# Kernel optimization log

Hardware: AMD Instinct MI355X
Metric: run time of the kernel (lower is better)

## Reference

```python
import jax, jax.numpy as jnp
import numpy as np

B, N, F_IN = 8, 2048, 16
E, H = 64, 4
D = E // H
HID, A = 128, 4
QUEUE_IDX = np.array([0, 1, 2, 3, 6, 7, 8, 9, 10, 11, 12, 13])


def setup_inputs() -> dict:
    key = jax.random.key(0)
    ks = iter(jax.random.split(key, 64))
    def g(*s, scale=0.05):
        return jax.random.normal(next(ks), s, jnp.float32) * scale
    inp = {}
    inp['node_features'] = jax.random.normal(next(ks), (B, N, F_IN), jnp.float32) * 10.0
    inp['adjacency'] = jax.random.randint(next(ks), (B, N, N), 0, 2).astype(jnp.float32)
    for i, fin in enumerate([F_IN, E]):
        inp[f'l{i}_wq'] = g(fin, E)
        inp[f'l{i}_wk'] = g(fin, E)
        inp[f'l{i}_wv'] = g(fin, E)
        inp[f'l{i}_in_w'] = g(E, 3 * E)
        inp[f'l{i}_in_b'] = jnp.zeros(3 * E, jnp.float32)
        inp[f'l{i}_mha_ow'] = g(E, E)
        inp[f'l{i}_mha_ob'] = jnp.zeros(E, jnp.float32)
        inp[f'l{i}_op_w'] = g(E, E)
        inp[f'l{i}_op_b'] = jnp.zeros(E, jnp.float32)
    inp['head_w1'] = g(E, HID)
    inp['head_b1'] = jnp.zeros(HID, jnp.float32)
    inp['head_w2'] = g(HID, HID)
    inp['head_b2'] = jnp.zeros(HID, jnp.float32)
    inp['head_w3'] = g(HID, A, scale=0.001)
    inp['head_b3'] = jnp.zeros(A, jnp.float32)
    return inp


def _gat_layer(x, mask, wq, wk, wv, in_w, in_b, mow, mob, opw, opb):
    # x: [B,N,Fin], mask: [B,N,N] bool (True = blocked)
    b, n, _ = x.shape
    q = x @ wq  # layer's own Q/K/V projections (bias-free)
    k = x @ wk
    v = x @ wv
    # nn.MultiheadAttention's internal in_proj (with bias)
    Q = q @ in_w[:, :E] + in_b[:E]
    K = k @ in_w[:, E:2 * E] + in_b[E:2 * E]
    V = v @ in_w[:, 2 * E:] + in_b[2 * E:]
    Qh = Q.reshape(b, n, H, D)
    Kh = K.reshape(b, n, H, D)
    Vh = V.reshape(b, n, H, D)
    s = jnp.einsum('bqhd,bkhd->bhqk', Qh, Kh) / jnp.sqrt(jnp.float32(D))
    s = jnp.where(mask[:, None, :, :], -jnp.inf, s)
    a = jax.nn.softmax(s, axis=-1)  # diagonal always unmasked -> no all-inf rows
    o = jnp.einsum('bhqk,bkhd->bqhd', a, Vh).reshape(b, n, E)
    o = o @ mow + mob  # MHA out_proj
    return o @ opw + opb  # layer out_proj


def reference(node_features, adjacency,
              l0_wq, l0_wk, l0_wv, l0_in_w, l0_in_b, l0_mha_ow, l0_mha_ob, l0_op_w, l0_op_b,
              l1_wq, l1_wk, l1_wv, l1_in_w, l1_in_b, l1_mha_ow, l1_mha_ob, l1_op_w, l1_op_b,
              head_w1, head_b1, head_w2, head_b2, head_w3, head_b3):
    f = node_features.shape[-1]
    scale = jnp.ones(f, node_features.dtype).at[QUEUE_IDX].set(1.0 / 50.0).at[5].set(1.0 / 300.0)
    x = node_features * scale
    n = adjacency.shape[-1]
    mask = (adjacency + jnp.eye(n, dtype=adjacency.dtype)) == 0
    x = jax.nn.relu(_gat_layer(x, mask, l0_wq, l0_wk, l0_wv, l0_in_w, l0_in_b, l0_mha_ow, l0_mha_ob, l0_op_w, l0_op_b))
    x = jax.nn.relu(_gat_layer(x, mask, l1_wq, l1_wk, l1_wv, l1_in_w, l1_in_b, l1_mha_ow, l1_mha_ob, l1_op_w, l1_op_b))
    h = jax.nn.relu(x @ head_w1 + head_b1)
    h = jax.nn.relu(h @ head_w2 + head_b2)
    return h @ head_w3 + head_b3  # [B, N, n_actions]
```

## Files before the change

### kernel.cpp

```cpp
#include <hip/hip_runtime.h>

#define BB 8
#define NN 2048
#define FIN0 16
#define EE 64
#define HH 4
#define DD 16
#define HIDN 128
#define AA 4

__global__ __launch_bounds__(256) void k_mask(const float* __restrict__ adj, unsigned long long* __restrict__ mbT) {
    const int ITER = 32;
    for (int it = 0; it < ITER; it++) {
        long long idx = ((long long)blockIdx.x * ITER + it) * 256 + threadIdx.x;
        int k = (int)(idx & (NN - 1));
        int r = (int)((idx >> 11) & (NN - 1));
        int b = (int)(idx >> 22);
        float a = adj[idx];
        bool blocked = (a == 0.0f) && (k != r);
        unsigned long long m = __ballot(blocked);
        if ((threadIdx.x & 63) == 0) mbT[((long long)b * 32 + (k >> 6)) * NN + r] = m;
    }
}

#define QSCALE 0.36067376022224085f
__device__ __forceinline__ float sfeat(int f) {
    return (f == 4 || f == 14 || f == 15) ? 1.0f : ((f == 5) ? (1.0f / 300.0f) : 0.02f);
}
__global__ __launch_bounds__(256) void k_wcomb(
        const float* __restrict__ wq0, const float* __restrict__ wk0, const float* __restrict__ wv0,
        const float* __restrict__ inw0, const float* __restrict__ inb0,
        const float* __restrict__ mow0, const float* __restrict__ mob0,
        const float* __restrict__ opw0, const float* __restrict__ opb0,
        const float* __restrict__ wq1, const float* __restrict__ wk1, const float* __restrict__ wv1,
        const float* __restrict__ inw1, const float* __restrict__ inb1,
        const float* __restrict__ mow1, const float* __restrict__ mob1,
        const float* __restrict__ opw1, const float* __restrict__ opb1,
        float* __restrict__ CW0, float* __restrict__ WO0, float* __restrict__ bO0, float* __restrict__ bQ0,
        float* __restrict__ CW1, float* __restrict__ WO1, float* __restrict__ bO1, float* __restrict__ bQ1) {
    int ly = blockIdx.y;
    int fin = ly ? EE : FIN0;
    const float* wq = ly ? wq1 : wq0; const float* wk = ly ? wk1 : wk0; const float* wv = ly ? wv1 : wv0;
    const float* inw = ly ? inw1 : inw0; const float* inb = ly ? inb1 : inb0;
    const float* mow = ly ? mow1 : mow0; const float* mob = ly ? mob1 : mob0;
    const float* opw = ly ? opw1 : opw0; const float* opb = ly ? opb1 : opb0;
    float* CW = ly ? CW1 : CW0; float* WO = ly ? WO1 : WO0;
    float* bO = ly ? bO1 : bO0; float* bQ = ly ? bQ1 : bQ0;

    int t = blockIdx.x * 256 + threadIdx.x;
    int t1 = fin * 192;
    int t2 = t1 + 4096;
    int t3 = t2 + 64;
    int t4 = t3 + 192;
    if (t < t1) {
        int f = t / 192, j = t % 192;
        const float* w = (j < 64) ? wq : ((j < 128) ? wk : wv);
        float acc = 0.f;
        for (int kk = 0; kk < 64; kk++) acc += w[f * 64 + kk] * inw[kk * 192 + j];
        if (j < 64) acc *= QSCALE;
        if (ly == 0) acc *= sfeat(f);
        CW[t] = acc;
    } else if (t < t2) {
        int u = t - t1; int i = u >> 6, j = u & 63;
        float acc = 0.f;
        for (int kk = 0; kk < 64; kk++) acc += mow[i * 64 + kk] * opw[kk * 64 + j];
        WO[u] = acc;
    } else if (t < t3) {
        int j = t - t2;
        float acc = opb[j];
        for (int kk = 0; kk < 64; kk++) acc += mob[kk] * opw[kk * 64 + j];
        bO[j] = acc;
    } else if (t < t4) {
        int j = t - t3;
        bQ[j] = inb[j] * ((j < 64) ? QSCALE : 1.0f);
    }
}

template <int FINP>
__global__ __launch_bounds__(256) void k_qkv(const float* __restrict__ X, const float* __restrict__ CW,
                                             const float* __restrict__ bQ,
                                             float* __restrict__ Q, float* __restrict__ K, float* __restrict__ V) {
    int lane = threadIdx.x & 63;
    int quarter = threadIdx.x >> 6;
    int row = blockIdx.x * 64 + lane;
    int b = row >> 11, n = row & (NN - 1);
    float xr[FINP];
    const float4* xp = (const float4*)(X + (long long)row * FINP);
#pragma unroll
    for (int i = 0; i < FINP / 4; i++) {
        float4 v = xp[i];
        xr[4 * i] = v.x; xr[4 * i + 1] = v.y; xr[4 * i + 2] = v.z; xr[4 * i + 3] = v.w;
    }
    for (int jq = 0; jq < 12; jq++) {
        int j = quarter * 48 + jq * 4;
        float4 acc = *(const float4*)(bQ + j);
#pragma unroll
        for (int f = 0; f < FINP; f++) {
            float4 w = *(const float4*)(CW + f * 192 + j);
            acc.x = fmaf(xr[f], w.x, acc.x);
            acc.y = fmaf(xr[f], w.y, acc.y);
            acc.z = fmaf(xr[f], w.z, acc.z);
            acc.w = fmaf(xr[f], w.w, acc.w);
        }
        int which = j >> 6, c = j & 63, h = c >> 4, d = c & 15;
        float* dst = (which == 0) ? Q : ((which == 1) ? K : V);
        *(float4*)(dst + (((long long)(b * HH + h) * NN + n) * DD + d)) = acc;
    }
}

__global__ __launch_bounds__(512, 2) void k_attn(const float* __restrict__ Q, const float* __restrict__ K,
                                                 const float* __restrict__ V,
                                                 const unsigned long long* __restrict__ mbT,
                                                 float* __restrict__ O) {
    __shared__ float smem[8 * 4 * 64 * 17];
    int lane = threadIdx.x & 63;
    int w = threadIdx.x >> 6;
    int qb = blockIdx.x, h = blockIdx.y, b = blockIdx.z;
    int qbase = qb * 256;

    const float* Qbh = Q + (long long)(b * HH + h) * NN * DD;
    const float* Kb  = K + (long long)(b * HH + h) * NN * DD;
    const float* Vb  = V + (long long)(b * HH + h) * NN * DD;
    const unsigned long long* mrow = mbT + (long long)b * 32 * NN;

    float4 qf[4][4];
#pragma unroll
    for (int rq = 0; rq < 4; rq++) {
        const float4* qp = (const float4*)(Qbh + (long long)(qbase + rq * 64 + lane) * DD);
#pragma unroll
        for (int j = 0; j < 4; j++) qf[rq][j] = qp[j];
    }
    float4 oacc[4][4];
#pragma unroll
    for (int rq = 0; rq < 4; rq++)
#pragma unroll
        for (int j = 0; j < 4; j++) oacc[rq][j] = make_float4(0.f, 0.f, 0.f, 0.f);
    float lsum[4] = {0.f, 0.f, 0.f, 0.f};

    float* sK = smem + w * 2048;
    float* sV = sK + 1024;

    float4 kpre[4], vpre[4];
    unsigned long long mwpre[4];
    {
        const float4* srcK = (const float4*)(Kb + (long long)(w * 256) * DD);
        const float4* srcV = (const float4*)(Vb + (long long)(w * 256) * DD);
#pragma unroll
        for (int i = 0; i < 4; i++) { kpre[i] = srcK[lane + 64 * i]; vpre[i] = srcV[lane + 64 * i]; }
#pragma unroll
        for (int rq = 0; rq < 4; rq++) mwpre[rq] = mrow[(long long)(w * 4) * NN + qbase + rq * 64 + lane];
    }

#pragma unroll
    for (int c = 0; c < 4; c++) {
#pragma unroll
        for (int i = 0; i < 4; i++) {
            ((float4*)sK)[lane + 64 * i] = kpre[i];
            ((float4*)sV)[lane + 64 * i] = vpre[i];
        }
        unsigned long long mw[4];
#pragma unroll
        for (int rq = 0; rq < 4; rq++) mw[rq] = mwpre[rq];
        if (c < 3) {
            int kcn = w * 256 + (c + 1) * 64;
            const float4* srcK = (const float4*)(Kb + (long long)kcn * DD);
            const float4* srcV = (const float4*)(Vb + (long long)kcn * DD);
#pragma unroll
            for (int i = 0; i < 4; i++) { kpre[i] = srcK[lane + 64 * i]; vpre[i] = srcV[lane + 64 * i]; }
            int kblkn = w * 4 + c + 1;
#pragma unroll
            for (int rq = 0; rq < 4; rq++) mwpre[rq] = mrow[(long long)kblkn * NN + qbase + rq * 64 + lane];
        }
        asm volatile("s_waitcnt lgkmcnt(0)" ::: "memory");
#pragma unroll 4
        for (int kk = 0; kk < 64; kk++) {
            const float4* kr = (const float4*)(sK + kk * 16);
            float4 k0 = kr[0], k1 = kr[1], k2 = kr[2], k3 = kr[3];
            float e[4];
#pragma unroll
            for (int rq = 0; rq < 4; rq++) {
                float4 a0 = qf[rq][0], a1 = qf[rq][1], a2 = qf[rq][2], a3 = qf[rq][3];
                float sA = a0.x * k0.x;
                sA = fmaf(a0.y, k0.y, sA); sA = fmaf(a0.z, k0.z, sA); sA = fmaf(a0.w, k0.w, sA);
                sA = fmaf(a1.x, k1.x, sA); sA = fmaf(a1.y, k1.y, sA); sA = fmaf(a1.z, k1.z, sA); sA = fmaf(a1.w, k1.w, sA);
                float sB = a2.x * k2.x;
                sB = fmaf(a2.y, k2.y, sB); sB = fmaf(a2.z, k2.z, sB); sB = fmaf(a2.w, k2.w, sB);
                sB = fmaf(a3.x, k3.x, sB); sB = fmaf(a3.y, k3.y, sB); sB = fmaf(a3.z, k3.z, sB); sB = fmaf(a3.w, k3.w, sB);
                float ee = __builtin_amdgcn_exp2f(sA + sB);
                e[rq] = ((mw[rq] >> kk) & 1ULL) ? 0.f : ee;
                lsum[rq] += e[rq];
            }
            const float4* vr = (const float4*)(sV + kk * 16);
            float4 v0 = vr[0], v1 = vr[1], v2 = vr[2], v3 = vr[3];
#pragma unroll
            for (int rq = 0; rq < 4; rq++) {
                float ew = e[rq];
                oacc[rq][0].x = fmaf(ew, v0.x, oacc[rq][0].x); oacc[rq][0].y = fmaf(ew, v0.y, oacc[rq][0].y);
                oacc[rq][0].z = fmaf(ew, v0.z, oacc[rq][0].z); oacc[rq][0].w = fmaf(ew, v0.w, oacc[rq][0].w);
                oacc[rq][1].x = fmaf(ew, v1.x, oacc[rq][1].x); oacc[rq][1].y = fmaf(ew, v1.y, oacc[rq][1].y);
                oacc[rq][1].z = fmaf(ew, v1.z, oacc[rq][1].z); oacc[rq][1].w = fmaf(ew, v1.w, oacc[rq][1].w);
                oacc[rq][2].x = fmaf(ew, v2.x, oacc[rq][2].x); oacc[rq][2].y = fmaf(ew, v2.y, oacc[rq][2].y);
                oacc[rq][2].z = fmaf(ew, v2.z, oacc[rq][2].z); oacc[rq][2].w = fmaf(ew, v2.w, oacc[rq][2].w);
                oacc[rq][3].x = fmaf(ew, v3.x, oacc[rq][3].x); oacc[rq][3].y = fmaf(ew, v3.y, oacc[rq][3].y);
                oacc[rq][3].z = fmaf(ew, v3.z, oacc[rq][3].z); oacc[rq][3].w = fmaf(ew, v3.w, oacc[rq][3].w);
            }
        }
    }
    __syncthreads();
#pragma unroll
    for (int rq = 0; rq < 4; rq++) {
        float* rp = smem + (((w * 4 + rq) * 64 + lane)) * 17;
#pragma unroll
        for (int j = 0; j < 4; j++) {
            rp[4 * j + 0] = oacc[rq][j].x; rp[4 * j + 1] = oacc[rq][j].y;
            rp[4 * j + 2] = oacc[rq][j].z; rp[4 * j + 3] = oacc[rq][j].w;
        }
        rp[16] = lsum[rq];
    }
    __syncthreads();
    if (w < 4) {
        int rq = w;
        float acc[DD]; float lt = 0.f;
#pragma unroll
        for (int d = 0; d < DD; d++) acc[d] = 0.f;
#pragma unroll
        for (int p = 0; p < 8; p++) {
            const float* pp = smem + (((p * 4 + rq) * 64 + lane)) * 17;
#pragma unroll
            for (int d = 0; d < DD; d++) acc[d] += pp[d];
            lt += pp[16];
        }
        float inv = 1.0f / lt;
        int q = qbase + rq * 64 + lane;
        float* op = O + (long long)(b * NN + q) * EE + h * DD;
        float4 r0 = {acc[0]*inv, acc[1]*inv, acc[2]*inv, acc[3]*inv};
        float4 r1 = {acc[4]*inv, acc[5]*inv, acc[6]*inv, acc[7]*inv};
        float4 r2 = {acc[8]*inv, acc[9]*inv, acc[10]*inv, acc[11]*inv};
        float4 r3 = {acc[12]*inv, acc[13]*inv, acc[14]*inv, acc[15]*inv};
        ((float4*)op)[0] = r0; ((float4*)op)[1] = r1; ((float4*)op)[2] = r2; ((float4*)op)[3] = r3;
    }
}

__global__ __launch_bounds__(256) void k_outqkv(const float* __restrict__ O, const float* __restrict__ WO,
                                                const float* __restrict__ bO,
                                                const float* __restrict__ CW, const float* __restrict__ bQ,
                                                float* __restrict__ Q, float* __restrict__ K, float* __restrict__ V) {
    __shared__ float xs[64 * 68];
    int lane = threadIdx.x & 63, quarter = threadIdx.x >> 6;
    long long row = (long long)blockIdx.x * 64 + lane;
    int b = (int)(row >> 11), n = (int)(row & (NN - 1));
    {
        float xr[64];
        const float4* xp = (const float4*)(O + row * 64);
#pragma unroll
        for (int i = 0; i < 16; i++) {
            float4 t = xp[i];
            xr[4 * i] = t.x; xr[4 * i + 1] = t.y; xr[4 * i + 2] = t.z; xr[4 * i + 3] = t.w;
        }
        for (int jq = 0; jq < 4; jq++) {
            int j = quarter * 16 + jq * 4;
            float4 acc = *(const float4*)(bO + j);
#pragma unroll
            for (int f = 0; f < 64; f++) {
                float4 w4 = *(const float4*)(WO + f * 64 + j);
                acc.x = fmaf(xr[f], w4.x, acc.x);
                acc.y = fmaf(xr[f], w4.y, acc.y);
                acc.z = fmaf(xr[f], w4.z, acc.z);
                acc.w = fmaf(xr[f], w4.w, acc.w);
            }
            acc.x = fmaxf(acc.x, 0.f); acc.y = fmaxf(acc.y, 0.f);
            acc.z = fmaxf(acc.z, 0.f); acc.w = fmaxf(acc.w, 0.f);
            *(float4*)(xs + lane * 68 + j) = acc;
        }
    }
    __syncthreads();
    {
        float xr[64];
        const float4* xp = (const float4*)(xs + lane * 68);
#pragma unroll
        for (int i = 0; i < 16; i++) {
            float4 t = xp[i];
            xr[4 * i] = t.x; xr[4 * i + 1] = t.y; xr[4 * i + 2] = t.z; xr[4 * i + 3] = t.w;
        }
        for (int jq = 0; jq < 12; jq++) {
            int j = quarter * 48 + jq * 4;
            float4 acc = *(const float4*)(bQ + j);
#pragma unroll
            for (int f = 0; f < 64; f++) {
                float4 w4 = *(const float4*)(CW + f * 192 + j);
                acc.x = fmaf(xr[f], w4.x, acc.x);
                acc.y = fmaf(xr[f], w4.y, acc.y);
                acc.z = fmaf(xr[f], w4.z, acc.z);
                acc.w = fmaf(xr[f], w4.w, acc.w);
            }
            int which = j >> 6, c = j & 63, h = c >> 4, d = c & 15;
            float* dst = (which == 0) ? Q : ((which == 1) ? K : V);
            *(float4*)(dst + (((long long)(b * HH + h) * NN + n) * DD + d)) = acc;
        }
    }
}

__global__ __launch_bounds__(128) void k_outhead(const float* __restrict__ O,
                                                 const float* __restrict__ WO, const float* __restrict__ bO,
                                                 const float* __restrict__ w1, const float* __restrict__ b1,
                                                 const float* __restrict__ w2, const float* __restrict__ b2,
                                                 const float* __restrict__ w3, const float* __restrict__ b3,
                                                 float* __restrict__ out) {
    __shared__ float Xs[16 * 64];
    __shared__ float X2s[16 * 68];
    __shared__ float H1[16 * 132];
    __shared__ float H2[16 * 132];
    int tid = threadIdx.x;
    long long row0 = (long long)blockIdx.x * 16;
    {
        const float4* src = (const float4*)(O + row0 * 64);
        float4* dst = (float4*)Xs;
        dst[tid] = src[tid];
        dst[tid + 128] = src[tid + 128];
    }
    __syncthreads();
    {
        int col = tid & 63;
        float wr[64];
#pragma unroll
        for (int f = 0; f < 64; f++) wr[f] = WO[f * 64 + col];
        float bb = bO[col];
#pragma unroll
        for (int rr = 0; rr < 8; rr++) {
            int r = (tid >> 6) * 8 + rr;
            const float4* x4 = (const float4*)(Xs + r * 64);
            float a0 = bb, a1 = 0.f, a2 = 0.f, a3 = 0.f;
#pragma unroll
            for (int fq = 0; fq < 16; fq++) {
                float4 xv = x4[fq];
                a0 = fmaf(xv.x, wr[4 * fq], a0);
                a1 = fmaf(xv.y, wr[4 * fq + 1], a1);
                a2 = fmaf(xv.z, wr[4 * fq + 2], a2);
                a3 = fmaf(xv.w, wr[4 * fq + 3], a3);
            }
            X2s[r * 68 + col] = fmaxf((a0 + a1) + (a2 + a3), 0.f);
        }
    }
    __syncthreads();
    {
        float wr[64];
#pragma unroll
        for (int f = 0; f < 64; f++) wr[f] = w1[f * 128 + tid];
        float bb = b1[tid];
        for (int r = 0; r < 16; r++) {
            const float4* x4 = (const float4*)(X2s + r * 68);
            float a0 = bb, a1 = 0.f, a2 = 0.f, a3 = 0.f;
#pragma unroll
            for (int fq = 0; fq < 16; fq++) {
                float4 xv = x4[fq];
                a0 = fmaf(xv.x, wr[4 * fq], a0);
                a1 = fmaf(xv.y, wr[4 * fq + 1], a1);
                a2 = fmaf(xv.z, wr[4 * fq + 2], a2);
                a3 = fmaf(xv.w, wr[4 * fq + 3], a3);
            }
            H1[r * 132 + tid] = fmaxf((a0 + a1) + (a2 + a3), 0.f);
        }
    }
    __syncthreads();
    {
        float acc2[16];
        float bb2 = b2[tid];
#pragma unroll
        for (int r = 0; r < 16; r++) acc2[r] = bb2;
#pragma unroll
        for (int p = 0; p < 2; p++) {
            float wr2[64];
#pragma unroll
            for (int i = 0; i < 64; i++) wr2[i] = w2[(p * 64 + i) * 128 + tid];
            for (int r = 0; r < 16; r++) {
                const float4* h4 = (const float4*)(H1 + r * 132 + p * 64);
                float a0 = 0.f, a1 = 0.f, a2 = 0.f, a3 = 0.f;
#pragma unroll
                for (int fq = 0; fq < 16; fq++) {
                    float4 xv = h4[fq];
                    a0 = fmaf(xv.x, wr2[4 * fq], a0);
                    a1 = fmaf(xv.y, wr2[4 * fq + 1], a1);
                    a2 = fmaf(xv.z, wr2[4 * fq + 2], a2);
                    a3 = fmaf(xv.w, wr2[4 * fq + 3], a3);
                }
                acc2[r] += (a0 + a1) + (a2 + a3);
            }
        }
#pragma unroll
        for (int r = 0; r < 16; r++) H2[r * 132 + tid] = fmaxf(acc2[r], 0.f);
    }
    __syncthreads();
    if (tid < 64) {
        int r = tid >> 2, a = tid & 3;
        float acc = b3[a];
        for (int f = 0; f < 128; f++) acc = fmaf(H2[r * 132 + f], w3[f * 4 + a], acc);
        out[(row0 + r) * 4 + a] = acc;
    }
}

extern "C" void kernel_launch(void* const* d_in, const int* in_sizes, int n_in,
                              void* d_out, int out_size, void* d_ws, size_t ws_size,
                              hipStream_t stream) {
    const float* nf = (const float*)d_in[0];
    const float* adj = (const float*)d_in[1];
    const float* l0[9]; for (int i = 0; i < 9; i++) l0[i] = (const float*)d_in[2 + i];
    const float* l1[9]; for (int i = 0; i < 9; i++) l1[i] = (const float*)d_in[11 + i];
    const float* hw1 = (const float*)d_in[20]; const float* hb1 = (const float*)d_in[21];
    const float* hw2 = (const float*)d_in[22]; const float* hb2 = (const float*)d_in[23];
    const float* hw3 = (const float*)d_in[24]; const float* hb3 = (const float*)d_in[25];
    float* out = (float*)d_out;

    char* ws = (char*)d_ws;
    size_t off = 0;
    auto alloc = [&](size_t bytes) -> void* {
        void* p = ws + off;
        off = (off + bytes + 255) & ~(size_t)255;
        return p;
    };
    unsigned long long* mbT = (unsigned long long*)alloc((size_t)BB * NN * NN / 8);
    float* Q = (float*)alloc((size_t)BB * HH * NN * DD * 4);
    float* K = (float*)alloc((size_t)BB * HH * NN * DD * 4);
    float* V = (float*)alloc((size_t)BB * HH * NN * DD * 4);
    float* O = (float*)alloc((size_t)BB * NN * EE * 4);
    float* CW0 = (float*)alloc(16 * 192 * 4);
    float* CW1 = (float*)alloc(64 * 192 * 4);
    float* WO0 = (float*)alloc(64 * 64 * 4);
    float* WO1 = (float*)alloc(64 * 64 * 4);
    float* bO0 = (float*)alloc(64 * 4);
    float* bO1 = (float*)alloc(64 * 4);
    float* bQ0 = (float*)alloc(192 * 4);
    float* bQ1 = (float*)alloc(192 * 4);

    k_mask<<<4096, 256, 0, stream>>>(adj, mbT);
    k_wcomb<<<dim3(65, 2), 256, 0, stream>>>(
        l0[0], l0[1], l0[2], l0[3], l0[4], l0[5], l0[6], l0[7], l0[8],
        l1[0], l1[1], l1[2], l1[3], l1[4], l1[5], l1[6], l1[7], l1[8],
        CW0, WO0, bO0, bQ0, CW1, WO1, bO1, bQ1);

    k_qkv<16><<<BB * NN / 64, 256, 0, stream>>>(nf, CW0, bQ0, Q, K, V);
    k_attn<<<dim3(NN / 256, HH, BB), 512, 0, stream>>>(Q, K, V, mbT, O);
    k_outqkv<<<BB * NN / 64, 256, 0, stream>>>(O, WO0, bO0, CW1, bQ1, Q, K, V);
    k_attn<<<dim3(NN / 256, HH, BB), 512, 0, stream>>>(Q, K, V, mbT, O);
    k_outhead<<<BB * NN / 16, 128, 0, stream>>>(O, WO1, bO1, hw1, hb1, hw2, hb2, hw3, hb3, out);
}
```

Measured before the change: 589.7 us.

## Split attention key range across two blocks and combine partials in consumers

```diff
diff --git a/kernel.cpp b/kernel.cpp
--- a/kernel.cpp
+++ b/kernel.cpp
@@ -111,11 +111,12 @@
 __global__ __launch_bounds__(512, 2) void k_attn(const float* __restrict__ Q, const float* __restrict__ K,
                                                  const float* __restrict__ V,
                                                  const unsigned long long* __restrict__ mbT,
-                                                 float* __restrict__ O) {
-    __shared__ float smem[8 * 4 * 64 * 17];
+                                                 float* __restrict__ Op, float* __restrict__ Lp) {
+    __shared__ float smem[16 * 64 * 17];
     int lane = threadIdx.x & 63;
     int w = threadIdx.x >> 6;
-    int qb = blockIdx.x, h = blockIdx.y, b = blockIdx.z;
+    int kh = blockIdx.x & 1, qb = blockIdx.x >> 1;
+    int h = blockIdx.y, b = blockIdx.z;
     int qbase = qb * 256;
 
     const float* Qbh = Q + (long long)(b * HH + h) * NN * DD;
@@ -139,20 +140,21 @@
 
     float* sK = smem + w * 2048;
     float* sV = sK + 1024;
+    int krow0 = kh * 1024 + w * 128;
 
     float4 kpre[4], vpre[4];
     unsigned long long mwpre[4];
     {
-        const float4* srcK = (const float4*)(Kb + (long long)(w * 256) * DD);
-        const float4* srcV = (const float4*)(Vb + (long long)(w * 256) * DD);
+        const float4* srcK = (const float4*)(Kb + (long long)krow0 * DD);
+        const float4* srcV = (const float4*)(Vb + (long long)krow0 * DD);
 #pragma unroll
         for (int i = 0; i < 4; i++) { kpre[i] = srcK[lane + 64 * i]; vpre[i] = srcV[lane + 64 * i]; }
 #pragma unroll
-        for (int rq = 0; rq < 4; rq++) mwpre[rq] = mrow[(long long)(w * 4) * NN + qbase + rq * 64 + lane];
-    }
-
-#pragma unroll
-    for (int c = 0; c < 4; c++) {
+        for (int rq = 0; rq < 4; rq++) mwpre[rq] = mrow[(long long)(krow0 >> 6) * NN + qbase + rq * 64 + lane];
+    }
+
+#pragma unroll
+    for (int c = 0; c < 2; c++) {
 #pragma unroll
         for (int i = 0; i < 4; i++) {
             ((float4*)sK)[lane + 64 * i] = kpre[i];
@@ -161,13 +163,15 @@
         unsigned long long mw[4];
 #pragma unroll
         for (int rq = 0; rq < 4; rq++) mw[rq] = mwpre[rq];
-        if (c < 3) {
-            int kcn = w * 256 + (c + 1) * 64;
+        if (c < 1) {
+            int kcn = krow0 + 64;
             const float4* srcK = (const float4*)(Kb + (long long)kcn * DD);
             const float4* srcV = (const float4*)(Vb + (long long)kcn * DD);
 #pragma unroll
             for (int i = 0; i < 4; i++) { kpre[i] = srcK[lane + 64 * i]; vpre[i] = srcV[lane + 64 * i]; }
-            int kblkn = w * 4 + c + 1;
+        }
+        {
+            int kblkn = (krow0 >> 6) + c + 1;
 #pragma unroll
             for (int rq = 0; rq < 4; rq++) mwpre[rq] = mrow[(long long)kblkn * NN + qbase + rq * 64 + lane];
         }
@@ -207,42 +211,74 @@
         }
     }
     __syncthreads();
-#pragma unroll
-    for (int rq = 0; rq < 4; rq++) {
-        float* rp = smem + (((w * 4 + rq) * 64 + lane)) * 17;
-#pragma unroll
-        for (int j = 0; j < 4; j++) {
-            rp[4 * j + 0] = oacc[rq][j].x; rp[4 * j + 1] = oacc[rq][j].y;
-            rp[4 * j + 2] = oacc[rq][j].z; rp[4 * j + 3] = oacc[rq][j].w;
-        }
-        rp[16] = lsum[rq];
+    if (w >= 4) {
+        int sw = w - 4;
+#pragma unroll
+        for (int rq = 0; rq < 4; rq++) {
+            float* rp = smem + (((sw * 4 + rq) * 64 + lane)) * 17;
+#pragma unroll
+            for (int j = 0; j < 4; j++) {
+                rp[4 * j + 0] = oacc[rq][j].x; rp[4 * j + 1] = oacc[rq][j].y;
+                rp[4 * j + 2] = oacc[rq][j].z; rp[4 * j + 3] = oacc[rq][j].w;
+            }
+            rp[16] = lsum[rq];
+        }
     }
     __syncthreads();
     if (w < 4) {
-        int rq = w;
-        float acc[DD]; float lt = 0.f;
-#pragma unroll
-        for (int d = 0; d < DD; d++) acc[d] = 0.f;
-#pragma unroll
-        for (int p = 0; p < 8; p++) {
-            const float* pp = smem + (((p * 4 + rq) * 64 + lane)) * 17;
-#pragma unroll
-            for (int d = 0; d < DD; d++) acc[d] += pp[d];
-            lt += pp[16];
-        }
-        float inv = 1.0f / lt;
-        int q = qbase + rq * 64 + lane;
-        float* op = O + (long long)(b * NN + q) * EE + h * DD;
-        float4 r0 = {acc[0]*inv, acc[1]*inv, acc[2]*inv, acc[3]*inv};
-        float4 r1 = {acc[4]*inv, acc[5]*inv, acc[6]*inv, acc[7]*inv};
-        float4 r2 = {acc[8]*inv, acc[9]*inv, acc[10]*inv, acc[11]*inv};
-        float4 r3 = {acc[12]*inv, acc[13]*inv, acc[14]*inv, acc[15]*inv};
-        ((float4*)op)[0] = r0; ((float4*)op)[1] = r1; ((float4*)op)[2] = r2; ((float4*)op)[3] = r3;
-    }
-}
-
-__global__ __launch_bounds__(256) void k_outqkv(const float* __restrict__ O, const float* __restrict__ WO,
-                                                const float* __restrict__ bO,
+#pragma unroll
+        for (int rq = 0; rq < 4; rq++) {
+            const float* pp = smem + (((w * 4 + rq) * 64 + lane)) * 17;
+#pragma unroll
+            for (int j = 0; j < 4; j++) {
+                oacc[rq][j].x += pp[4 * j + 0]; oacc[rq][j].y += pp[4 * j + 1];
+                oacc[rq][j].z += pp[4 * j + 2]; oacc[rq][j].w += pp[4 * j + 3];
+            }
+            lsum[rq] += pp[16];
+        }
+    }
+    __syncthreads();
+    if (w >= 1 && w < 4) {
+        int sw = w - 1;
+#pragma unroll
+        for (int rq = 0; rq < 4; rq++) {
+            float* rp = smem + (((sw * 4 + rq) * 64 + lane)) * 17;
+#pragma unroll
+            for (int j = 0; j < 4; j++) {
+                rp[4 * j + 0] = oacc[rq][j].x; rp[4 * j + 1] = oacc[rq][j].y;
+                rp[4 * j + 2] = oacc[rq][j].z; rp[4 * j + 3] = oacc[rq][j].w;
+            }
+            rp[16] = lsum[rq];
+        }
+    }
+    __syncthreads();
+    if (w == 0) {
+#pragma unroll
+        for (int p = 0; p < 3; p++) {
+#pragma unroll
+            for (int rq = 0; rq < 4; rq++) {
+                const float* pp = smem + (((p * 4 + rq) * 64 + lane)) * 17;
+#pragma unroll
+                for (int j = 0; j < 4; j++) {
+                    oacc[rq][j].x += pp[4 * j + 0]; oacc[rq][j].y += pp[4 * j + 1];
+                    oacc[rq][j].z += pp[4 * j + 2]; oacc[rq][j].w += pp[4 * j + 3];
+                }
+                lsum[rq] += pp[16];
+            }
+        }
+#pragma unroll
+        for (int rq = 0; rq < 4; rq++) {
+            int q = qbase + rq * 64 + lane;
+            float* op = Op + (((long long)kh * BB + b) * NN + q) * EE + h * DD;
+#pragma unroll
+            for (int j = 0; j < 4; j++) ((float4*)op)[j] = oacc[rq][j];
+            Lp[(((long long)kh * BB + b) * NN + q) * HH + h] = lsum[rq];
+        }
+    }
+}
+
+__global__ __launch_bounds__(256) void k_outqkv(const float* __restrict__ Op, const float* __restrict__ Lp,
+                                                const float* __restrict__ WO, const float* __restrict__ bO,
                                                 const float* __restrict__ CW, const float* __restrict__ bQ,
                                                 float* __restrict__ Q, float* __restrict__ K, float* __restrict__ V) {
     __shared__ float xs[64 * 68];
@@ -250,12 +286,19 @@
     long long row = (long long)blockIdx.x * 64 + lane;
     int b = (int)(row >> 11), n = (int)(row & (NN - 1));
     {
+        float linv[4];
+#pragma unroll
+        for (int h2 = 0; h2 < 4; h2++)
+            linv[h2] = 1.0f / (Lp[row * 4 + h2] + Lp[(long long)BB * NN * HH + row * 4 + h2]);
         float xr[64];
-        const float4* xp = (const float4*)(O + row * 64);
+        const float4* xp0 = (const float4*)(Op + row * 64);
+        const float4* xp1 = (const float4*)(Op + (long long)BB * NN * EE + row * 64);
 #pragma unroll
         for (int i = 0; i < 16; i++) {
-            float4 t = xp[i];
-            xr[4 * i] = t.x; xr[4 * i + 1] = t.y; xr[4 * i + 2] = t.z; xr[4 * i + 3] = t.w;
+            float4 t0 = xp0[i], t1 = xp1[i];
+            float s = linv[i >> 2];
+            xr[4 * i] = (t0.x + t1.x) * s; xr[4 * i + 1] = (t0.y + t1.y) * s;
+            xr[4 * i + 2] = (t0.z + t1.z) * s; xr[4 * i + 3] = (t0.w + t1.w) * s;
         }
         for (int jq = 0; jq < 4; jq++) {
             int j = quarter * 16 + jq * 4;
@@ -300,7 +343,7 @@
     }
 }
 
-__global__ __launch_bounds__(128) void k_outhead(const float* __restrict__ O,
+__global__ __launch_bounds__(128) void k_outhead(const float* __restrict__ Op, const float* __restrict__ Lp,
                                                  const float* __restrict__ WO, const float* __restrict__ bO,
                                                  const float* __restrict__ w1, const float* __restrict__ b1,
                                                  const float* __restrict__ w2, const float* __restrict__ b2,
@@ -312,11 +355,16 @@
     __shared__ float H2[16 * 132];
     int tid = threadIdx.x;
     long long row0 = (long long)blockIdx.x * 16;
-    {
-        const float4* src = (const float4*)(O + row0 * 64);
-        float4* dst = (float4*)Xs;
-        dst[tid] = src[tid];
-        dst[tid + 128] = src[tid + 128];
+#pragma unroll
+    for (int uu = 0; uu < 2; uu++) {
+        int u = tid + uu * 128;
+        int r = u >> 4, cq = u & 15;
+        long long rw = row0 + r;
+        float4 t0 = ((const float4*)(Op + rw * 64))[cq];
+        float4 t1 = ((const float4*)(Op + (long long)BB * NN * EE + rw * 64))[cq];
+        float inv = 1.0f / (Lp[rw * 4 + (cq >> 2)] + Lp[(long long)BB * NN * HH + rw * 4 + (cq >> 2)]);
+        float4 cmb = {(t0.x + t1.x) * inv, (t0.y + t1.y) * inv, (t0.z + t1.z) * inv, (t0.w + t1.w) * inv};
+        ((float4*)Xs)[u] = cmb;
     }
     __syncthreads();
     {
@@ -421,7 +469,8 @@
     float* Q = (float*)alloc((size_t)BB * HH * NN * DD * 4);
     float* K = (float*)alloc((size_t)BB * HH * NN * DD * 4);
     float* V = (float*)alloc((size_t)BB * HH * NN * DD * 4);
-    float* O = (float*)alloc((size_t)BB * NN * EE * 4);
+    float* Op = (float*)alloc((size_t)2 * BB * NN * EE * 4);
+    float* Lp = (float*)alloc((size_t)2 * BB * NN * HH * 4);
     float* CW0 = (float*)alloc(16 * 192 * 4);
     float* CW1 = (float*)alloc(64 * 192 * 4);
     float* WO0 = (float*)alloc(64 * 64 * 4);
@@ -438,8 +487,8 @@
         CW0, WO0, bO0, bQ0, CW1, WO1, bO1, bQ1);
 
     k_qkv<16><<<BB * NN / 64, 256, 0, stream>>>(nf, CW0, bQ0, Q, K, V);
-    k_attn<<<dim3(NN / 256, HH, BB), 512, 0, stream>>>(Q, K, V, mbT, O);
-    k_outqkv<<<BB * NN / 64, 256, 0, stream>>>(O, WO0, bO0, CW1, bQ1, Q, K, V);
-    k_attn<<<dim3(NN / 256, HH, BB), 512, 0, stream>>>(Q, K, V, mbT, O);
-    k_outhead<<<BB * NN / 16, 128, 0, stream>>>(O, WO1, bO1, hw1, hb1, hw2, hb2, hw3, hb3, out);
-}
+    k_attn<<<dim3(2 * NN / 256, HH, BB), 512, 0, stream>>>(Q, K, V, mbT, Op, Lp);
+    k_outqkv<<<BB * NN / 64, 256, 0, stream>>>(Op, Lp, WO0, bO0, CW1, bQ1, Q, K, V);
+    k_attn<<<dim3(2 * NN / 256, HH, BB), 512, 0, stream>>>(Q, K, V, mbT, Op, Lp);
+    k_outhead<<<BB * NN / 16, 128, 0, stream>>>(Op, Lp, WO1, bO1, hw1, hb1, hw2, hb2, hw3, hb3, out);
+}
```

After: 627.0 us. 1.06x slower.
